# Kernel optimization log

Hardware: AMD Instinct MI355X
Metric: run time of the kernel (lower is better)

## Reference

```python
import jax, jax.numpy as jnp
import numpy as np

N_NODES = 50000
N_EDGES = 800000
IN_CH = 128
HID = 64
N_GRAPHS = 512


def setup_inputs() -> dict:
    key = jax.random.key(0)
    ks = jax.random.split(key, 16)
    s = 0.05
    x = jax.random.normal(ks[0], (N_NODES, IN_CH), dtype=jnp.float32)
    edge_index = jax.random.randint(ks[1], (2, N_EDGES), 0, N_NODES, dtype=jnp.int32)
    batch = jnp.sort(jax.random.randint(ks[2], (N_NODES,), 0, N_GRAPHS, dtype=jnp.int32))
    return {
        "x": x,
        "edge_index": edge_index,
        "batch": batch,
        # GraphConv layer 1: lin_rel (weight+bias) applied to aggregated neighbors, lin_root (no bias)
        "W_rel1": jax.random.normal(ks[3], (IN_CH, HID), dtype=jnp.float32) * s,
        "b_rel1": jnp.zeros((HID,), dtype=jnp.float32),
        "W_root1": jax.random.normal(ks[4], (IN_CH, HID), dtype=jnp.float32) * s,
        "W_rel2": jax.random.normal(ks[5], (HID, HID), dtype=jnp.float32) * s,
        "b_rel2": jnp.zeros((HID,), dtype=jnp.float32),
        "W_root2": jax.random.normal(ks[6], (HID, HID), dtype=jnp.float32) * s,
        "W_rel3": jax.random.normal(ks[7], (HID, HID), dtype=jnp.float32) * s,
        "b_rel3": jnp.zeros((HID,), dtype=jnp.float32),
        "W_root3": jax.random.normal(ks[8], (HID, HID), dtype=jnp.float32) * s,
        "W_fc1": jax.random.normal(ks[9], (HID, 32), dtype=jnp.float32) * s,
        "b_fc1": jnp.zeros((32,), dtype=jnp.float32),
        "W_fc2": jax.random.normal(ks[10], (32, 1), dtype=jnp.float32) * s,
        "b_fc2": jnp.zeros((1,), dtype=jnp.float32),
    }


def reference(x, edge_index, batch,
              W_rel1, b_rel1, W_root1,
              W_rel2, b_rel2, W_root2,
              W_rel3, b_rel3, W_root3,
              W_fc1, b_fc1, W_fc2, b_fc2):
    src, dst = edge_index[0], edge_index[1]  # messages flow src -> dst

    def graph_conv(h, W_rel, b_rel, W_root):
        # PyG GraphConv: out = lin_rel(sum_{j in N(i)} h_j) + lin_root(h_i)
        agg = jax.ops.segment_sum(h[src], dst, num_segments=N_NODES)  # [N, d]
        return agg @ W_rel + b_rel + h @ W_root

    h = jax.nn.relu(graph_conv(x, W_rel1, b_rel1, W_root1))
    h = jax.nn.relu(graph_conv(h, W_rel2, b_rel2, W_root2))
    h = jax.nn.relu(graph_conv(h, W_rel3, b_rel3, W_root3))

    # global_mean_pool over graphs in the batch
    sums = jax.ops.segment_sum(h, batch, num_segments=N_GRAPHS)          # [G, 64]
    cnts = jax.ops.segment_sum(jnp.ones((h.shape[0], 1), h.dtype), batch,
                               num_segments=N_GRAPHS)                     # [G, 1]
    pooled = sums / jnp.maximum(cnts, 1.0)

    out = jax.nn.relu(pooled @ W_fc1 + b_fc1)
    return (out @ W_fc2 + b_fc2).reshape(-1)  # [G]
```

## Files before the change

### kernel.cpp

```cpp
#include <hip/hip_runtime.h>
#include <cstdint>
#include <cstddef>

#define NN 50000
#define NE 800000
#define GRAPHS 512
#define NBK 782
#define CAP 2048
#define GG1 782

typedef __attribute__((ext_vector_type(8))) short bf16x8;
typedef __attribute__((ext_vector_type(4))) float f32x4;
typedef __attribute__((ext_vector_type(2))) float f32x2;

__device__ __forceinline__ unsigned short f2bf(float f) {
  union { float f; unsigned u; } v; v.f = f;
  unsigned r = v.u + 0x7FFF + ((v.u >> 16) & 1);
  return (unsigned short)(r >> 16);
}
__device__ __forceinline__ float bf2f(unsigned short h) {
  union { unsigned u; float f; } v; v.u = ((unsigned)h) << 16;
  return v.f;
}

__device__ __forceinline__ unsigned char f2fp8_sw(float f) {
  union { float f; unsigned u; } v; v.f = f;
  unsigned s = (v.u >> 24) & 0x80;
  unsigned u = v.u & 0x7fffffffu;
  if (u < 0x3c000000u) {
    float a = fabsf(f) * 512.0f;
    int mi = (int)(a + 0.5f); if (mi > 7) mi = 7;
    return (unsigned char)(s | mi);
  }
  unsigned r = u + 0x7FFFF + ((u >> 20) & 1);
  int e = (int)(r >> 23) - 127;
  unsigned m = (r >> 20) & 7;
  if (e > 8) { e = 8; m = 6; }
  return (unsigned char)(s | ((unsigned)(e + 7) << 3) | m);
}
__device__ __forceinline__ float fp82f_sw(unsigned b) {
  unsigned s = (b & 0x80) << 24;
  unsigned e = (b >> 3) & 0xF, m = b & 7;
  union { unsigned u; float f; } v;
  if (e == 0) {
    float sub = (float)m * 0.001953125f;
    return (b & 0x80) ? -sub : sub;
  }
  v.u = s | ((e + 120) << 23) | (m << 20);
  return v.f;
}
__device__ __forceinline__ void fp8pair(float a, float b,
                                        unsigned char& c0, unsigned char& c1) {
#if __has_builtin(__builtin_amdgcn_cvt_pk_fp8_f32)
  int p = __builtin_amdgcn_cvt_pk_fp8_f32(a, b, 0, false);
  c0 = (unsigned char)(p & 0xFF); c1 = (unsigned char)((p >> 8) & 0xFF);
#else
  c0 = f2fp8_sw(a); c1 = f2fp8_sw(b);
#endif
}
__device__ __forceinline__ float4 fp8x4_dec(unsigned u) {
#if __has_builtin(__builtin_amdgcn_cvt_pk_f32_fp8)
  f32x2 lo = __builtin_amdgcn_cvt_pk_f32_fp8((int)u, false);
  f32x2 hi = __builtin_amdgcn_cvt_pk_f32_fp8((int)u, true);
  return make_float4(lo[0], lo[1], hi[0], hi[1]);
#else
  return make_float4(fp82f_sw(u & 0xFF), fp82f_sw((u >> 8) & 0xFF),
                     fp82f_sw((u >> 16) & 0xFF), fp82f_sw((u >> 24) & 0xFF));
#endif
}

__global__ __launch_bounds__(256) void setup_kernel(
    const int* __restrict__ batch, int* __restrict__ gstart,
    int* __restrict__ bcnt, float* __restrict__ pooled,
    const float* __restrict__ Wrel1, const float* __restrict__ Wroot1,
    const float* __restrict__ Wrel2, const float* __restrict__ Wroot2,
    const float* __restrict__ Wrel3, const float* __restrict__ Wroot3,
    unsigned short* __restrict__ Wt1, unsigned short* __restrict__ Wt2,
    unsigned short* __restrict__ Wt3) {
  const int tid = blockIdx.x * 256 + threadIdx.x;
  const int stride = gridDim.x * 256;
  for (int i = tid; i < NBK; i += stride) bcnt[i] = 0;
  for (int i = tid; i < GRAPHS * 64; i += stride) pooled[i] = 0.f;
  for (int g = tid; g <= GRAPHS; g += stride) {
    int lo = 0, hi = NN;
    while (lo < hi) {
      int mid = (lo + hi) >> 1;
      if (batch[mid] < g) lo = mid + 1; else hi = mid;
    }
    gstart[g] = lo;
  }
  for (int idx = tid; idx < 128 * 128; idx += stride) {
    int c = idx >> 7, k = idx & 127;
    Wt1[c * 128 + k] = f2bf(c < 64 ? Wrel1[k * 64 + c] : Wroot1[k * 64 + (c - 64)]);
  }
  for (int idx = tid; idx < 128 * 64; idx += stride) {
    int c = idx >> 6, k = idx & 63;
    Wt2[c * 64 + k] = f2bf(c < 64 ? Wrel2[k * 64 + c] : Wroot2[k * 64 + (c - 64)]);
    Wt3[c * 64 + k] = f2bf(c < 64 ? Wrel3[k * 64 + c] : Wroot3[k * 64 + (c - 64)]);
  }
}

__global__ __launch_bounds__(256) void bin_gemm1_kernel(
    const float* __restrict__ h, const unsigned short* __restrict__ Wt,
    const float* __restrict__ brel,
    unsigned char* __restrict__ hW, unsigned short* __restrict__ root,
    const int* __restrict__ src, const int* __restrict__ dst,
    int* __restrict__ bcnt, unsigned* __restrict__ ebuf) {
  __shared__ __align__(16) char smem[32768];
  const int t = threadIdx.x;

  if (blockIdx.x < GG1) {
    constexpr int K = 128;
    unsigned short* bs = (unsigned short*)smem;
    constexpr int SEG = K / 8;
    const int row0 = blockIdx.x * 64;

    for (int idx = t; idx < 128 * SEG; idx += 256) {
      int c = idx / SEG, kq = idx % SEG;
      uint4 v = *(const uint4*)&Wt[c * K + kq * 8];
      int sidx = (c * K + kq * 8) ^ ((c & 7) << 3);
      *(uint4*)&bs[sidx] = v;
    }

    const int lane = t & 63, wave = t >> 6;
    const int li = lane & 15;
    const int kg = (lane >> 4) * 8;
    const int ar_node = row0 + wave * 16 + li;
    const bool valid = ar_node < NN;

    bf16x8 af[4];
    #pragma unroll
    for (int i = 0; i < 4; ++i) {
      float4 v0 = make_float4(0.f, 0.f, 0.f, 0.f), v1 = v0;
      if (valid) {
        const float* p = &h[(size_t)ar_node * K + i * 32 + kg];
        v0 = *(const float4*)p; v1 = *(const float4*)(p + 4);
      }
      union { bf16x8 b; uint4 u; } pk;
      pk.u.x = f2bf(v0.x) | ((unsigned)f2bf(v0.y) << 16);
      pk.u.y = f2bf(v0.z) | ((unsigned)f2bf(v0.w) << 16);
      pk.u.z = f2bf(v1.x) | ((unsigned)f2bf(v1.y) << 16);
      pk.u.w = f2bf(v1.z) | ((unsigned)f2bf(v1.w) << 16);
      af[i] = pk.b;
    }
    __syncthreads();

    f32x4 acc[8];
    #pragma unroll
    for (int i = 0; i < 8; ++i) acc[i] = (f32x4){0.f, 0.f, 0.f, 0.f};

    #pragma unroll
    for (int i = 0; i < 4; ++i) {
      int ka = i * 32 + kg;
      #pragma unroll
      for (int nb = 0; nb < 8; ++nb) {
        int bc = nb * 16 + li;
        bf16x8 b = *(bf16x8*)&bs[(bc * K + ka) ^ ((bc & 7) << 3)];
        acc[nb] = __builtin_amdgcn_mfma_f32_16x16x32_bf16(af[i], b, acc[nb], 0, 0, 0);
      }
    }

    const int orow = row0 + wave * 16 + (lane >> 4) * 4;
    #pragma unroll
    for (int nb = 0; nb < 4; ++nb) {
      unsigned char cb[4];
      fp8pair(acc[nb][0], acc[nb][1], cb[0], cb[1]);
      fp8pair(acc[nb][2], acc[nb][3], cb[2], cb[3]);
      #pragma unroll
      for (int r = 0; r < 4; ++r) {
        int node = orow + r;
        if (node < NN) hW[(size_t)node * 64 + nb * 16 + li] = cb[r];
      }
    }
    #pragma unroll
    for (int nb = 4; nb < 8; ++nb) {
      float bb = brel[(nb - 4) * 16 + li];
      #pragma unroll
      for (int r = 0; r < 4; ++r) {
        int node = orow + r;
        if (node < NN) root[(size_t)node * 64 + (nb - 4) * 16 + li] = f2bf(acc[nb][r] + bb);
      }
    }
  } else {
    int* hist = (int*)smem;
    int* base = hist + NBK;
    int* lcur = base + NBK;
    for (int b = t; b < NBK; b += 256) { hist[b] = 0; lcur[b] = 0; }
    __syncthreads();
    const int e0 = (blockIdx.x - GG1) * 4096;
    unsigned pk[16]; int bk[16];
    #pragma unroll
    for (int i = 0; i < 16; ++i) {
      int e = e0 + i * 256 + t;
      if (e < NE) {
        int s = src[e], d = dst[e];
        bk[i] = d >> 6;
        pk[i] = ((unsigned)(d & 63) << 17) | (unsigned)s;
        atomicAdd(&hist[bk[i]], 1);
      } else bk[i] = -1;
    }
    __syncthreads();
    for (int b = t; b < NBK; b += 256) {
      int c = hist[b];
      if (c) base[b] = atomicAdd(&bcnt[b], c);
    }
    __syncthreads();
    #pragma unroll
    for (int i = 0; i < 16; ++i) {
      if (bk[i] >= 0) {
        int r = atomicAdd(&lcur[bk[i]], 1);
        ebuf[(size_t)bk[i] * CAP + base[bk[i]] + r] = pk[i];
      }
    }
  }
}

__global__ __launch_bounds__(256) void bucket_csr_kernel(const unsigned* __restrict__ ebuf,
                                                         const int* __restrict__ bcnt,
                                                         int* __restrict__ rs,
                                                         int* __restrict__ ren,
                                                         unsigned short* __restrict__ ssrc) {
  __shared__ int ehist[64];
  __shared__ int sd[64];
  __shared__ int ecur[64];
  const int t = threadIdx.x;
  const int b = blockIdx.x;
  const int n0 = b << 6;
  const int e0 = b * CAP;
  const int cnt = bcnt[b];
  if (t < 64) ehist[t] = 0;
  __syncthreads();
  for (int e = t; e < cnt; e += 256)
    atomicAdd(&ehist[ebuf[e0 + e] >> 17], 1);
  __syncthreads();
  if (t < 64) sd[t] = ehist[t];
  __syncthreads();
  for (int off = 1; off < 64; off <<= 1) {
    int u = (t >= off && t < 64) ? sd[t - off] : 0;
    __syncthreads();
    if (t < 64) sd[t] += u;
    __syncthreads();
  }
  if (t < 64) {
    int ex = e0 + sd[t] - ehist[t];
    ecur[t] = ex;
    rs[n0 + t] = ex;
    ren[n0 + t] = e0 + sd[t];
  }
  __syncthreads();
  for (int e = t; e < cnt; e += 256) {
    unsigned ed = ebuf[e0 + e];
    int r = atomicAdd(&ecur[ed >> 17], 1);
    ssrc[r] = (unsigned short)(ed & 0xFFFF);
  }
}

__device__ __forceinline__ float4 gather_node(
    const unsigned short* __restrict__ rootPrev,
    const unsigned char* __restrict__ hWp,
    const unsigned short* __restrict__ ssrc,
    int node, int c4, int s0, int s1) {
  ushort4 rt = *(const ushort4*)&rootPrev[(size_t)node * 64 + c4];
  float4 a0 = make_float4(bf2f(rt.x), bf2f(rt.y), bf2f(rt.z), bf2f(rt.w));
  float4 a1 = make_float4(0.f, 0.f, 0.f, 0.f);
  float4 a2 = make_float4(0.f, 0.f, 0.f, 0.f);
  float4 a3 = make_float4(0.f, 0.f, 0.f, 0.f);
  int e = s0;
  for (; e + 4 <= s1; e += 4) {
    unsigned uA = *(const unsigned*)&hWp[(size_t)ssrc[e] * 64 + c4];
    unsigned uB = *(const unsigned*)&hWp[(size_t)ssrc[e + 1] * 64 + c4];
    unsigned uC = *(const unsigned*)&hWp[(size_t)ssrc[e + 2] * 64 + c4];
    unsigned uD = *(const unsigned*)&hWp[(size_t)ssrc[e + 3] * 64 + c4];
    float4 vA = fp8x4_dec(uA), vB = fp8x4_dec(uB);
    float4 vC = fp8x4_dec(uC), vD = fp8x4_dec(uD);
    a0.x += vA.x; a0.y += vA.y; a0.z += vA.z; a0.w += vA.w;
    a1.x += vB.x; a1.y += vB.y; a1.z += vB.z; a1.w += vB.w;
    a2.x += vC.x; a2.y += vC.y; a2.z += vC.z; a2.w += vC.w;
    a3.x += vD.x; a3.y += vD.y; a3.z += vD.z; a3.w += vD.w;
  }
  for (; e < s1; ++e) {
    unsigned uA = *(const unsigned*)&hWp[(size_t)ssrc[e] * 64 + c4];
    float4 vA = fp8x4_dec(uA);
    a0.x += vA.x; a0.y += vA.y; a0.z += vA.z; a0.w += vA.w;
  }
  a0.x += a1.x + a2.x + a3.x; a0.y += a1.y + a2.y + a3.y;
  a0.z += a1.z + a2.z + a3.z; a0.w += a1.w + a2.w + a3.w;
  return a0;
}

__global__ __launch_bounds__(256) void agg_gemm_kernel(
    const unsigned short* __restrict__ rootPrev,
    const unsigned char* __restrict__ hWp,
    const int* __restrict__ rs, const int* __restrict__ ren,
    const unsigned short* __restrict__ ssrc,
    const unsigned short* __restrict__ Wt,
    const float* __restrict__ brel,
    unsigned char* __restrict__ hW,
    unsigned short* __restrict__ rootOut) {
  __shared__ __align__(16) unsigned short as[16 * 64];
  __shared__ __align__(16) unsigned short bs[128 * 64];
  const int t = threadIdx.x;
  const int n0 = blockIdx.x * 16;

  #pragma unroll
  for (int i = 0; i < 4; ++i) {
    int idx = t + i * 256;
    int c = idx >> 3, kq = idx & 7;
    uint4 v = *(const uint4*)&Wt[c * 64 + kq * 8];
    int sidx = (c * 64 + kq * 8) ^ ((c & 7) << 3);
    *(uint4*)&bs[sidx] = v;
  }

  const int r = t >> 4, l16 = t & 15, c4 = l16 * 4;
  const int node = n0 + r;
  float4 a0 = gather_node(rootPrev, hWp, ssrc, node, c4, rs[node], ren[node]);
  a0.x = fmaxf(a0.x, 0.f); a0.y = fmaxf(a0.y, 0.f);
  a0.z = fmaxf(a0.z, 0.f); a0.w = fmaxf(a0.w, 0.f);
  uint2 p;
  p.x = f2bf(a0.x) | ((unsigned)f2bf(a0.y) << 16);
  p.y = f2bf(a0.z) | ((unsigned)f2bf(a0.w) << 16);
  *(uint2*)&as[(r * 64 + c4) ^ ((r & 7) << 3)] = p;
  __syncthreads();

  const int lane = t & 63, wave = t >> 6;
  const int li = lane & 15, kg = (lane >> 4) * 8;
  f32x4 acc[2];
  acc[0] = (f32x4){0.f, 0.f, 0.f, 0.f};
  acc[1] = (f32x4){0.f, 0.f, 0.f, 0.f};
  #pragma unroll
  for (int ks = 0; ks < 2; ++ks) {
    int ka = ks * 32 + kg;
    bf16x8 a = *(bf16x8*)&as[(li * 64 + ka) ^ ((li & 7) << 3)];
    #pragma unroll
    for (int nb = 0; nb < 2; ++nb) {
      int bc = wave * 32 + nb * 16 + li;
      bf16x8 b = *(bf16x8*)&bs[(bc * 64 + ka) ^ ((bc & 7) << 3)];
      acc[nb] = __builtin_amdgcn_mfma_f32_16x16x32_bf16(a, b, acc[nb], 0, 0, 0);
    }
  }

  const int orow = n0 + (lane >> 4) * 4;
  if (wave < 2) {
    #pragma unroll
    for (int nb = 0; nb < 2; ++nb) {
      int col = wave * 32 + nb * 16 + li;
      unsigned char cb[4];
      fp8pair(acc[nb][0], acc[nb][1], cb[0], cb[1]);
      fp8pair(acc[nb][2], acc[nb][3], cb[2], cb[3]);
      #pragma unroll
      for (int rr = 0; rr < 4; ++rr)
        hW[(size_t)(orow + rr) * 64 + col] = cb[rr];
    }
  } else {
    #pragma unroll
    for (int nb = 0; nb < 2; ++nb) {
      int col = (wave - 2) * 32 + nb * 16 + li;
      float bb = brel[col];
      #pragma unroll
      for (int rr = 0; rr < 4; ++rr)
        rootOut[(size_t)(orow + rr) * 64 + col] = f2bf(acc[nb][rr] + bb);
    }
  }
}

__global__ __launch_bounds__(256) void agg_pool_kernel(
    const unsigned short* __restrict__ rootPrev,
    const unsigned char* __restrict__ hWp,
    const int* __restrict__ rs, const int* __restrict__ ren,
    const unsigned short* __restrict__ ssrc,
    const int* __restrict__ batch,
    float* __restrict__ pooled) {
  __shared__ float h3s[16 * 64];
  __shared__ int batch_s[16];
  const int t = threadIdx.x;
  const int n0 = blockIdx.x * 16;
  if (t < 16) batch_s[t] = batch[n0 + t];

  const int r = t >> 4, l16 = t & 15, c4 = l16 * 4;
  const int node = n0 + r;
  float4 a0 = gather_node(rootPrev, hWp, ssrc, node, c4, rs[node], ren[node]);
  float4 o;
  o.x = fmaxf(a0.x, 0.f); o.y = fmaxf(a0.y, 0.f);
  o.z = fmaxf(a0.z, 0.f); o.w = fmaxf(a0.w, 0.f);
  *(float4*)&h3s[r * 64 + c4] = o;
  __syncthreads();

  if (t < 64) {
    int cur = batch_s[0]; float acc = 0.f;
    #pragma unroll
    for (int rr = 0; rr < 16; ++rr) {
      int g = batch_s[rr];
      if (g != cur) {
        unsafeAtomicAdd(&pooled[cur * 64 + t], acc);
        acc = 0.f; cur = g;
      }
      acc += h3s[rr * 64 + t];
    }
    unsafeAtomicAdd(&pooled[cur * 64 + t], acc);
  }
}

__global__ __launch_bounds__(64) void head_kernel(
    const float* __restrict__ pooled, const int* __restrict__ gstart,
    const float* __restrict__ Wfc1, const float* __restrict__ bfc1,
    const float* __restrict__ Wfc2, const float* __restrict__ bfc2,
    float* __restrict__ out) {
  __shared__ float m[64];
  __shared__ float h1[32];
  const int g = blockIdx.x, l = threadIdx.x;
  float c = fmaxf((float)(gstart[g + 1] - gstart[g]), 1.0f);
  m[l] = pooled[g * 64 + l] / c;
  __syncthreads();
  if (l < 32) {
    float a = bfc1[l];
    #pragma unroll
    for (int k = 0; k < 64; ++k) a += m[k] * Wfc1[k * 32 + l];
    h1[l] = fmaxf(a, 0.f);
  }
  __syncthreads();
  if (l == 0) {
    float o = bfc2[0];
    #pragma unroll
    for (int j = 0; j < 32; ++j) o += h1[j] * Wfc2[j];
    out[g] = o;
  }
}

extern "C" void kernel_launch(void* const* d_in, const int* in_sizes, int n_in,
                              void* d_out, int out_size, void* d_ws, size_t ws_size,
                              hipStream_t stream) {
  const float* x      = (const float*)d_in[0];
  const int*   ei     = (const int*)d_in[1];
  const int*   batch  = (const int*)d_in[2];
  const float* Wrel1  = (const float*)d_in[3];
  const float* brel1  = (const float*)d_in[4];
  const float* Wroot1 = (const float*)d_in[5];
  const float* Wrel2  = (const float*)d_in[6];
  const float* brel2  = (const float*)d_in[7];
  const float* Wroot2 = (const float*)d_in[8];
  const float* Wrel3  = (const float*)d_in[9];
  const float* brel3  = (const float*)d_in[10];
  const float* Wroot3 = (const float*)d_in[11];
  const float* Wfc1   = (const float*)d_in[12];
  const float* bfc1   = (const float*)d_in[13];
  const float* Wfc2   = (const float*)d_in[14];
  const float* bfc2   = (const float*)d_in[15];
  const int* src = ei;
  const int* dst = ei + NE;

  char* w = (char*)d_ws;
  auto alloc = [&](size_t bytes) -> char* {
    char* p = w; w += (bytes + 255) & ~(size_t)255; return p;
  };
  unsigned char*  hWa   = (unsigned char*)alloc((size_t)NN * 64);
  unsigned char*  hWb   = (unsigned char*)alloc((size_t)NN * 64);
  unsigned short* rootA = (unsigned short*)alloc((size_t)NN * 64 * 2);
  unsigned short* rootB = (unsigned short*)alloc((size_t)NN * 64 * 2);
  int*   rs     = (int*)alloc((size_t)NBK * 64 * 4);
  int*   ren    = (int*)alloc((size_t)NBK * 64 * 4);
  unsigned short* ssrc = (unsigned short*)alloc((size_t)NBK * CAP * 2);
  int*   gstart = (int*)alloc((size_t)(GRAPHS + 1) * 4);
  int*   bcnt   = (int*)alloc((size_t)NBK * 4);
  float* pooled = (float*)alloc((size_t)GRAPHS * 64 * 4);
  unsigned* ebuf = (unsigned*)alloc((size_t)NBK * CAP * 4);
  unsigned short* Wt1 = (unsigned short*)alloc((size_t)128 * 128 * 2);
  unsigned short* Wt2 = (unsigned short*)alloc((size_t)128 * 64 * 2);
  unsigned short* Wt3 = (unsigned short*)alloc((size_t)128 * 64 * 2);

  setup_kernel<<<64, 256, 0, stream>>>(batch, gstart, bcnt, pooled,
                                       Wrel1, Wroot1, Wrel2, Wroot2, Wrel3, Wroot3,
                                       Wt1, Wt2, Wt3);
  bin_gemm1_kernel<<<GG1 + (NE + 4095) / 4096, 256, 0, stream>>>(
      x, Wt1, brel1, hWa, rootA, src, dst, bcnt, ebuf);
  bucket_csr_kernel<<<NBK, 256, 0, stream>>>(ebuf, bcnt, rs, ren, ssrc);

  agg_gemm_kernel<<<NN / 16, 256, 0, stream>>>(rootA, hWa, rs, ren, ssrc,
                                               Wt2, brel2, hWb, rootB);
  agg_gemm_kernel<<<NN / 16, 256, 0, stream>>>(rootB, hWb, rs, ren, ssrc,
                                               Wt3, brel3, hWa, rootA);
  agg_pool_kernel<<<NN / 16, 256, 0, stream>>>(rootA, hWa, rs, ren, ssrc,
                                               batch, pooled);
  head_kernel<<<GRAPHS, 64, 0, stream>>>(pooled, gstart, Wfc1, bfc1, Wfc2, bfc2,
                                         (float*)d_out);
}
```

Baseline: 91.59 us.

## Widen per-thread gather to 16 channels and process 64 nodes per block

The aggregation kernels now give each thread 16 channels of one node, using 16-byte fp8 loads, instead of 4 channels with 4-byte loads. Each block now covers 64 nodes with 4 threads per node, so every wave runs a 16x128 MFMA tile and the block loads the weight tile once for 64 nodes instead of 16. The aim is fewer, wider memory transactions and less repeated weight staging per node. In exchange, each node's edge loop is spread over only 4 lanes, so per-lane serial work and register pressure rise and degree imbalance inside a wave grows. Bounds checks are added for the partial last block.

New measurement: 104.6 us. 1.14x slower.

```diff
diff --git a/kernel.cpp b/kernel.cpp
--- a/kernel.cpp
+++ b/kernel.cpp
@@ -21,6 +21,12 @@
 __device__ __forceinline__ float bf2f(unsigned short h) {
   union { unsigned u; float f; } v; v.u = ((unsigned)h) << 16;
   return v.f;
+}
+__device__ __forceinline__ float4 bfq(unsigned lo, unsigned hi) {
+  return make_float4(bf2f((unsigned short)(lo & 0xFFFF)),
+                     bf2f((unsigned short)(lo >> 16)),
+                     bf2f((unsigned short)(hi & 0xFFFF)),
+                     bf2f((unsigned short)(hi >> 16)));
 }
 
 __device__ __forceinline__ unsigned char f2fp8_sw(float f) {
@@ -67,6 +73,39 @@
   return make_float4(fp82f_sw(u & 0xFF), fp82f_sw((u >> 8) & 0xFF),
                      fp82f_sw((u >> 16) & 0xFF), fp82f_sw((u >> 24) & 0xFF));
 #endif
+}
+__device__ __forceinline__ void add16(uint4 u, float4* a) {
+  float4 v0 = fp8x4_dec(u.x), v1 = fp8x4_dec(u.y);
+  float4 v2 = fp8x4_dec(u.z), v3 = fp8x4_dec(u.w);
+  a[0].x += v0.x; a[0].y += v0.y; a[0].z += v0.z; a[0].w += v0.w;
+  a[1].x += v1.x; a[1].y += v1.y; a[1].z += v1.z; a[1].w += v1.w;
+  a[2].x += v2.x; a[2].y += v2.y; a[2].z += v2.z; a[2].w += v2.w;
+  a[3].x += v3.x; a[3].y += v3.y; a[3].z += v3.z; a[3].w += v3.w;
+}
+
+__device__ __forceinline__ void gather16(
+    const unsigned short* __restrict__ rootPrev,
+    const unsigned char* __restrict__ hWp,
+    const unsigned short* __restrict__ ssrc,
+    const int* __restrict__ rs, const int* __restrict__ ren,
+    int node, int c16, float4* a) {
+  uint4 r0 = *(const uint4*)&rootPrev[(size_t)node * 64 + c16];
+  uint4 r1 = *(const uint4*)&rootPrev[(size_t)node * 64 + c16 + 8];
+  a[0] = bfq(r0.x, r0.y); a[1] = bfq(r0.z, r0.w);
+  a[2] = bfq(r1.x, r1.y); a[3] = bfq(r1.z, r1.w);
+  int e = rs[node];
+  const int s1 = ren[node];
+  for (; e + 4 <= s1; e += 4) {
+    uint4 u0 = *(const uint4*)&hWp[(size_t)ssrc[e]     * 64 + c16];
+    uint4 u1 = *(const uint4*)&hWp[(size_t)ssrc[e + 1] * 64 + c16];
+    uint4 u2 = *(const uint4*)&hWp[(size_t)ssrc[e + 2] * 64 + c16];
+    uint4 u3 = *(const uint4*)&hWp[(size_t)ssrc[e + 3] * 64 + c16];
+    add16(u0, a); add16(u1, a); add16(u2, a); add16(u3, a);
+  }
+  for (; e < s1; ++e) {
+    uint4 u0 = *(const uint4*)&hWp[(size_t)ssrc[e] * 64 + c16];
+    add16(u0, a);
+  }
 }
 
 __global__ __launch_bounds__(256) void setup_kernel(
@@ -255,39 +294,6 @@
   }
 }
 
-__device__ __forceinline__ float4 gather_node(
-    const unsigned short* __restrict__ rootPrev,
-    const unsigned char* __restrict__ hWp,
-    const unsigned short* __restrict__ ssrc,
-    int node, int c4, int s0, int s1) {
-  ushort4 rt = *(const ushort4*)&rootPrev[(size_t)node * 64 + c4];
-  float4 a0 = make_float4(bf2f(rt.x), bf2f(rt.y), bf2f(rt.z), bf2f(rt.w));
-  float4 a1 = make_float4(0.f, 0.f, 0.f, 0.f);
-  float4 a2 = make_float4(0.f, 0.f, 0.f, 0.f);
-  float4 a3 = make_float4(0.f, 0.f, 0.f, 0.f);
-  int e = s0;
-  for (; e + 4 <= s1; e += 4) {
-    unsigned uA = *(const unsigned*)&hWp[(size_t)ssrc[e] * 64 + c4];
-    unsigned uB = *(const unsigned*)&hWp[(size_t)ssrc[e + 1] * 64 + c4];
-    unsigned uC = *(const unsigned*)&hWp[(size_t)ssrc[e + 2] * 64 + c4];
-    unsigned uD = *(const unsigned*)&hWp[(size_t)ssrc[e + 3] * 64 + c4];
-    float4 vA = fp8x4_dec(uA), vB = fp8x4_dec(uB);
-    float4 vC = fp8x4_dec(uC), vD = fp8x4_dec(uD);
-    a0.x += vA.x; a0.y += vA.y; a0.z += vA.z; a0.w += vA.w;
-    a1.x += vB.x; a1.y += vB.y; a1.z += vB.z; a1.w += vB.w;
-    a2.x += vC.x; a2.y += vC.y; a2.z += vC.z; a2.w += vC.w;
-    a3.x += vD.x; a3.y += vD.y; a3.z += vD.z; a3.w += vD.w;
-  }
-  for (; e < s1; ++e) {
-    unsigned uA = *(const unsigned*)&hWp[(size_t)ssrc[e] * 64 + c4];
-    float4 vA = fp8x4_dec(uA);
-    a0.x += vA.x; a0.y += vA.y; a0.z += vA.z; a0.w += vA.w;
-  }
-  a0.x += a1.x + a2.x + a3.x; a0.y += a1.y + a2.y + a3.y;
-  a0.z += a1.z + a2.z + a3.z; a0.w += a1.w + a2.w + a3.w;
-  return a0;
-}
-
 __global__ __launch_bounds__(256) void agg_gemm_kernel(
     const unsigned short* __restrict__ rootPrev,
     const unsigned char* __restrict__ hWp,
@@ -297,10 +303,10 @@
     const float* __restrict__ brel,
     unsigned char* __restrict__ hW,
     unsigned short* __restrict__ rootOut) {
-  __shared__ __align__(16) unsigned short as[16 * 64];
+  __shared__ __align__(16) unsigned short as[64 * 64];
   __shared__ __align__(16) unsigned short bs[128 * 64];
   const int t = threadIdx.x;
-  const int n0 = blockIdx.x * 16;
+  const int n0 = blockIdx.x * 64;
 
   #pragma unroll
   for (int i = 0; i < 4; ++i) {
@@ -311,54 +317,65 @@
     *(uint4*)&bs[sidx] = v;
   }
 
-  const int r = t >> 4, l16 = t & 15, c4 = l16 * 4;
+  const int r = t >> 2, c16 = (t & 3) * 16;
   const int node = n0 + r;
-  float4 a0 = gather_node(rootPrev, hWp, ssrc, node, c4, rs[node], ren[node]);
-  a0.x = fmaxf(a0.x, 0.f); a0.y = fmaxf(a0.y, 0.f);
-  a0.z = fmaxf(a0.z, 0.f); a0.w = fmaxf(a0.w, 0.f);
-  uint2 p;
-  p.x = f2bf(a0.x) | ((unsigned)f2bf(a0.y) << 16);
-  p.y = f2bf(a0.z) | ((unsigned)f2bf(a0.w) << 16);
-  *(uint2*)&as[(r * 64 + c4) ^ ((r & 7) << 3)] = p;
+  float4 a[4];
+  if (node < NN) {
+    gather16(rootPrev, hWp, ssrc, rs, ren, node, c16, a);
+  } else {
+    a[0] = a[1] = a[2] = a[3] = make_float4(0.f, 0.f, 0.f, 0.f);
+  }
+  uint4 p0, p1;
+  p0.x = f2bf(fmaxf(a[0].x, 0.f)) | ((unsigned)f2bf(fmaxf(a[0].y, 0.f)) << 16);
+  p0.y = f2bf(fmaxf(a[0].z, 0.f)) | ((unsigned)f2bf(fmaxf(a[0].w, 0.f)) << 16);
+  p0.z = f2bf(fmaxf(a[1].x, 0.f)) | ((unsigned)f2bf(fmaxf(a[1].y, 0.f)) << 16);
+  p0.w = f2bf(fmaxf(a[1].z, 0.f)) | ((unsigned)f2bf(fmaxf(a[1].w, 0.f)) << 16);
+  p1.x = f2bf(fmaxf(a[2].x, 0.f)) | ((unsigned)f2bf(fmaxf(a[2].y, 0.f)) << 16);
+  p1.y = f2bf(fmaxf(a[2].z, 0.f)) | ((unsigned)f2bf(fmaxf(a[2].w, 0.f)) << 16);
+  p1.z = f2bf(fmaxf(a[3].x, 0.f)) | ((unsigned)f2bf(fmaxf(a[3].y, 0.f)) << 16);
+  p1.w = f2bf(fmaxf(a[3].z, 0.f)) | ((unsigned)f2bf(fmaxf(a[3].w, 0.f)) << 16);
+  *(uint4*)&as[(r * 64 + c16) ^ ((r & 7) << 3)] = p0;
+  *(uint4*)&as[(r * 64 + c16 + 8) ^ ((r & 7) << 3)] = p1;
   __syncthreads();
 
   const int lane = t & 63, wave = t >> 6;
   const int li = lane & 15, kg = (lane >> 4) * 8;
-  f32x4 acc[2];
-  acc[0] = (f32x4){0.f, 0.f, 0.f, 0.f};
-  acc[1] = (f32x4){0.f, 0.f, 0.f, 0.f};
+  const int ar = wave * 16 + li;
+  f32x4 acc[8];
+  #pragma unroll
+  for (int i = 0; i < 8; ++i) acc[i] = (f32x4){0.f, 0.f, 0.f, 0.f};
+
   #pragma unroll
   for (int ks = 0; ks < 2; ++ks) {
     int ka = ks * 32 + kg;
-    bf16x8 a = *(bf16x8*)&as[(li * 64 + ka) ^ ((li & 7) << 3)];
-    #pragma unroll
-    for (int nb = 0; nb < 2; ++nb) {
-      int bc = wave * 32 + nb * 16 + li;
-      bf16x8 b = *(bf16x8*)&bs[(bc * 64 + ka) ^ ((bc & 7) << 3)];
-      acc[nb] = __builtin_amdgcn_mfma_f32_16x16x32_bf16(a, b, acc[nb], 0, 0, 0);
-    }
-  }
-
-  const int orow = n0 + (lane >> 4) * 4;
-  if (wave < 2) {
-    #pragma unroll
-    for (int nb = 0; nb < 2; ++nb) {
-      int col = wave * 32 + nb * 16 + li;
-      unsigned char cb[4];
-      fp8pair(acc[nb][0], acc[nb][1], cb[0], cb[1]);
-      fp8pair(acc[nb][2], acc[nb][3], cb[2], cb[3]);
-      #pragma unroll
-      for (int rr = 0; rr < 4; ++rr)
-        hW[(size_t)(orow + rr) * 64 + col] = cb[rr];
-    }
-  } else {
-    #pragma unroll
-    for (int nb = 0; nb < 2; ++nb) {
-      int col = (wave - 2) * 32 + nb * 16 + li;
-      float bb = brel[col];
-      #pragma unroll
-      for (int rr = 0; rr < 4; ++rr)
-        rootOut[(size_t)(orow + rr) * 64 + col] = f2bf(acc[nb][rr] + bb);
+    bf16x8 av = *(bf16x8*)&as[(ar * 64 + ka) ^ ((ar & 7) << 3)];
+    #pragma unroll
+    for (int nb = 0; nb < 8; ++nb) {
+      int bc = nb * 16 + li;
+      bf16x8 bv = *(bf16x8*)&bs[(bc * 64 + ka) ^ ((bc & 7) << 3)];
+      acc[nb] = __builtin_amdgcn_mfma_f32_16x16x32_bf16(av, bv, acc[nb], 0, 0, 0);
+    }
+  }
+
+  const int orow = n0 + wave * 16 + (lane >> 4) * 4;
+  #pragma unroll
+  for (int nb = 0; nb < 4; ++nb) {
+    unsigned char cb[4];
+    fp8pair(acc[nb][0], acc[nb][1], cb[0], cb[1]);
+    fp8pair(acc[nb][2], acc[nb][3], cb[2], cb[3]);
+    #pragma unroll
+    for (int rr = 0; rr < 4; ++rr) {
+      int nd = orow + rr;
+      if (nd < NN) hW[(size_t)nd * 64 + nb * 16 + li] = cb[rr];
+    }
+  }
+  #pragma unroll
+  for (int nb = 4; nb < 8; ++nb) {
+    float bb = brel[(nb - 4) * 16 + li];
+    #pragma unroll
+    for (int rr = 0; rr < 4; ++rr) {
+      int nd = orow + rr;
+      if (nd < NN) rootOut[(size_t)nd * 64 + (nb - 4) * 16 + li] = f2bf(acc[nb][rr] + bb);
     }
   }
 }
@@ -370,25 +387,40 @@
     const unsigned short* __restrict__ ssrc,
     const int* __restrict__ batch,
     float* __restrict__ pooled) {
-  __shared__ float h3s[16 * 64];
-  __shared__ int batch_s[16];
+  __shared__ float h3s[64 * 64];
+  __shared__ int batch_s[64];
   const int t = threadIdx.x;
-  const int n0 = blockIdx.x * 16;
-  if (t < 16) batch_s[t] = batch[n0 + t];
-
-  const int r = t >> 4, l16 = t & 15, c4 = l16 * 4;
+  const int n0 = blockIdx.x * 64;
+  if (t < 64) {
+    int nd = n0 + t;
+    batch_s[t] = batch[nd < NN ? nd : (NN - 1)];
+  }
+
+  const int r = t >> 2, c16 = (t & 3) * 16;
   const int node = n0 + r;
-  float4 a0 = gather_node(rootPrev, hWp, ssrc, node, c4, rs[node], ren[node]);
-  float4 o;
-  o.x = fmaxf(a0.x, 0.f); o.y = fmaxf(a0.y, 0.f);
-  o.z = fmaxf(a0.z, 0.f); o.w = fmaxf(a0.w, 0.f);
-  *(float4*)&h3s[r * 64 + c4] = o;
+  float4 a[4];
+  if (node < NN) {
+    gather16(rootPrev, hWp, ssrc, rs, ren, node, c16, a);
+    a[0].x = fmaxf(a[0].x, 0.f); a[0].y = fmaxf(a[0].y, 0.f);
+    a[0].z = fmaxf(a[0].z, 0.f); a[0].w = fmaxf(a[0].w, 0.f);
+    a[1].x = fmaxf(a[1].x, 0.f); a[1].y = fmaxf(a[1].y, 0.f);
+    a[1].z = fmaxf(a[1].z, 0.f); a[1].w = fmaxf(a[1].w, 0.f);
+    a[2].x = fmaxf(a[2].x, 0.f); a[2].y = fmaxf(a[2].y, 0.f);
+    a[2].z = fmaxf(a[2].z, 0.f); a[2].w = fmaxf(a[2].w, 0.f);
+    a[3].x = fmaxf(a[3].x, 0.f); a[3].y = fmaxf(a[3].y, 0.f);
+    a[3].z = fmaxf(a[3].z, 0.f); a[3].w = fmaxf(a[3].w, 0.f);
+  } else {
+    a[0] = a[1] = a[2] = a[3] = make_float4(0.f, 0.f, 0.f, 0.f);
+  }
+  *(float4*)&h3s[r * 64 + c16]      = a[0];
+  *(float4*)&h3s[r * 64 + c16 + 4]  = a[1];
+  *(float4*)&h3s[r * 64 + c16 + 8]  = a[2];
+  *(float4*)&h3s[r * 64 + c16 + 12] = a[3];
   __syncthreads();
 
   if (t < 64) {
     int cur = batch_s[0]; float acc = 0.f;
-    #pragma unroll
-    for (int rr = 0; rr < 16; ++rr) {
+    for (int rr = 0; rr < 64; ++rr) {
       int g = batch_s[rr];
       if (g != cur) {
         unsafeAtomicAdd(&pooled[cur * 64 + t], acc);
@@ -474,12 +506,12 @@
       x, Wt1, brel1, hWa, rootA, src, dst, bcnt, ebuf);
   bucket_csr_kernel<<<NBK, 256, 0, stream>>>(ebuf, bcnt, rs, ren, ssrc);
 
-  agg_gemm_kernel<<<NN / 16, 256, 0, stream>>>(rootA, hWa, rs, ren, ssrc,
-                                               Wt2, brel2, hWb, rootB);
-  agg_gemm_kernel<<<NN / 16, 256, 0, stream>>>(rootB, hWb, rs, ren, ssrc,
-                                               Wt3, brel3, hWa, rootA);
-  agg_pool_kernel<<<NN / 16, 256, 0, stream>>>(rootA, hWa, rs, ren, ssrc,
-                                               batch, pooled);
+  agg_gemm_kernel<<<NBK, 256, 0, stream>>>(rootA, hWa, rs, ren, ssrc,
+                                           Wt2, brel2, hWb, rootB);
+  agg_gemm_kernel<<<NBK, 256, 0, stream>>>(rootB, hWb, rs, ren, ssrc,
+                                           Wt3, brel3, hWa, rootA);
+  agg_pool_kernel<<<NBK, 256, 0, stream>>>(rootA, hWa, rs, ren, ssrc,
+                                           batch, pooled);
   head_kernel<<<GRAPHS, 64, 0, stream>>>(pooled, gstart, Wfc1, bfc1, Wfc2, bfc2,
                                          (float*)d_out);
 }
```
